# Kernel tuning notes

Hardware: AMD Instinct MI355X
Metric: run time of the kernel (lower is better)

## Reference

```python
import jax, jax.numpy as jnp
import numpy as np

DIM = 2048
N_HEADS = 32
N_KV_HEADS = 4
HEAD_DIM = DIM // N_HEADS  # 64


def _rope_tables(T, head_dim, dtype):
    inv_freq = 1.0 / (10000.0 ** (jnp.arange(0, head_dim, 2, dtype=jnp.float32) / head_dim))
    t = jnp.arange(T, dtype=jnp.float32)
    freqs = jnp.einsum('i,j->ij', t, inv_freq)           # [T, head_dim/2]
    emb = jnp.concatenate([freqs, freqs], axis=-1)        # [T, head_dim]
    return jnp.cos(emb).astype(dtype), jnp.sin(emb).astype(dtype)


def _rotate_half(x):
    d = x.shape[-1] // 2
    return jnp.concatenate([-x[..., d:], x[..., :d]], axis=-1)


def setup_inputs() -> dict:
    key = jax.random.key(0)
    kx, kq, kk, kv, ko = jax.random.split(key, 5)
    s = 1.0 / np.sqrt(DIM)
    return {
        'x': jax.random.normal(kx, (2, 2048, DIM), dtype=jnp.float32),
        'wq': jax.random.normal(kq, (DIM, DIM), dtype=jnp.float32) * s,
        'wk': jax.random.normal(kk, (DIM, DIM // 8), dtype=jnp.float32) * s,
        'wv': jax.random.normal(kv, (DIM, DIM // 8), dtype=jnp.float32) * s,
        'wo': jax.random.normal(ko, (DIM, DIM), dtype=jnp.float32) * s,
    }


def reference(x, wq, wk, wv, wo):
    B, T, C = x.shape
    q = (x @ wq).reshape(B, T, N_HEADS, HEAD_DIM).transpose(0, 2, 1, 3)      # [B,H,T,D]
    k = (x @ wk).reshape(B, T, N_KV_HEADS, HEAD_DIM).transpose(0, 2, 1, 3)   # [B,Hkv,T,D]
    v = (x @ wv).reshape(B, T, N_KV_HEADS, HEAD_DIM).transpose(0, 2, 1, 3)

    cos, sin = _rope_tables(T, HEAD_DIM, x.dtype)  # [T,D]
    q = q * cos + _rotate_half(q) * sin
    k = k * cos + _rotate_half(k) * sin

    rep = N_HEADS // N_KV_HEADS
    k = jnp.repeat(k, rep, axis=1)  # [B,H,T,D]
    v = jnp.repeat(v, rep, axis=1)

    scale = 1.0 / np.sqrt(HEAD_DIM)
    scores = jnp.einsum('bhqd,bhkd->bhqk', q, k) * scale
    causal = jnp.tril(jnp.ones((T, T), dtype=bool))
    scores = jnp.where(causal, scores, jnp.finfo(scores.dtype).min)
    attn = jax.nn.softmax(scores, axis=-1)
    out = jnp.einsum('bhqk,bhkd->bhqd', attn, v)
    out = out.transpose(0, 2, 1, 3).reshape(B, T, C)
    return out @ wo
```

## Files before the change

kernel.cpp:

```cpp
#include <hip/hip_runtime.h>
#include <hip/hip_bf16.h>
#include <stdint.h>

#define DIM 2048
#define TSEQ 2048
#define BATCH 2
#define NH 32
#define NKV 4
#define HD 64
#define MROWS (BATCH*TSEQ)
#define NQKV 2560

typedef __attribute__((ext_vector_type(4))) float f32x4;
typedef __attribute__((ext_vector_type(8))) __bf16 bf16x8;
typedef unsigned short ushort_t;

#define GLDS16(g, l) __builtin_amdgcn_global_load_lds( \
    (const __attribute__((address_space(1))) void*)(g), \
    (__attribute__((address_space(3))) void*)(l), 16, 0, 0)

__device__ __forceinline__ float bflo2f(unsigned int w) {
  union { unsigned int i; float f; } c; c.i = w << 16; return c.f;
}
__device__ __forceinline__ unsigned short f2bf(float f) {
  union { float f; unsigned int i; } c; c.f = f;
  unsigned int x = c.i;
  x += 0x7fffu + ((x >> 16) & 1u);
  return (unsigned short)(x >> 16);
}
__device__ __forceinline__ unsigned short f2bf_fast(float f) {
  union { float f; unsigned int i; } c; c.f = f;
  return (unsigned short)((c.i + 0x8000u) >> 16);
}

#define LOG1E4_D32 0.2878231366242557f
#define QSCALE 0.1803368801111243f
#define PREP_CAST 8192
#define PREP_TC   (PREP_CAST + 9216)
#define PREP_TAB  (PREP_TC + 256)

__global__ void prep_all(const float* __restrict__ x, ushort_t* __restrict__ xb,
                         const float* __restrict__ wq, const float* __restrict__ wk,
                         const float* __restrict__ wv, const float* __restrict__ wo,
                         ushort_t* __restrict__ wtq, ushort_t* __restrict__ woT,
                         float2* __restrict__ tab) {
  __shared__ float tile[32][33];
  const int bid = blockIdx.x;
  if (bid < PREP_CAST) {
    const int i = bid * 256 + threadIdx.x;
    const float4 v = ((const float4*)x)[i];
    uint2 p;
    p.x = (unsigned int)f2bf(v.x) | ((unsigned int)f2bf(v.y) << 16);
    p.y = (unsigned int)f2bf(v.z) | ((unsigned int)f2bf(v.w) << 16);
    ((uint2*)xb)[i] = p;
  } else if (bid < PREP_TC) {
    const int tb = bid - PREP_CAST;
    const int by = tb >> 6;
    const float* src; ushort_t* dst; int N, bnb;
    if (by < 64)      { src = wq; dst = wtq;                    N = DIM; bnb = by; }
    else if (by < 72) { src = wk; dst = wtq + (long)DIM  * DIM; N = 256; bnb = by - 64; }
    else if (by < 80) { src = wv; dst = wtq + (long)2304 * DIM; N = 256; bnb = by - 72; }
    else              { src = wo; dst = woT;                    N = DIM; bnb = by - 80; }
    const int bk = (tb & 63) * 32;
    const int bn = bnb * 32;
    const int tx = threadIdx.x & 31;
    const int ty = threadIdx.x >> 5;
#pragma unroll
    for (int p = 0; p < 4; p++) {
      const int r = ty + p * 8;
      tile[r][tx] = src[(long)(bk + r) * N + bn + tx];
    }
    __syncthreads();
#pragma unroll
    for (int p = 0; p < 4; p++) {
      const int r = ty + p * 8;
      dst[(long)(bn + r) * DIM + bk + tx] = f2bf(tile[tx][r]);
    }
  } else {
    const int i = (bid - PREP_TC) * 256 + threadIdx.x;
    const int t = i >> 5, d = i & 31;
    const float ang = (float)t * __expf(-(float)d * LOG1E4_D32);
    float s_, c_;
    __sincosf(ang, &s_, &c_);
    tab[i] = make_float2(c_, s_);
  }
}

template<int EPI>
__global__ __launch_bounds__(256, 4) void gemm_bt(
    const ushort_t* __restrict__ A, const ushort_t* __restrict__ BT,
    int M, int N, int K,
    float* __restrict__ Cf, ushort_t* __restrict__ Cq,
    ushort_t* __restrict__ Ck, ushort_t* __restrict__ Cv,
    const float2* __restrict__ tab)
{
  __shared__ __align__(16) ushort_t As[128][64];
  __shared__ __align__(16) ushort_t Bs[128][64];
  const int tid  = threadIdx.x;
  const int lane = tid & 63;
  const int wid  = tid >> 6;
  const int wm   = wid >> 1, wn = wid & 1;
  const int l8   = lane >> 3;
  const int c8   = (lane & 7) * 8;

  const int nwg = (int)(gridDim.x * gridDim.y);
  const int bid = (int)(blockIdx.y * gridDim.x + blockIdx.x);
  const int swz = (bid & 7) * (nwg >> 3) + (bid >> 3);
  const int bx  = swz & 31;
  const int by  = swz >> 5;

  const long abase = (long)bx * 128 * K;
  const long bbase = (long)by * 128 * K;
  const int rsel = lane & 15;
  const int koff = (lane >> 4) * 8;
  f32x4 acc[4][4] = {};

  for (int k0 = 0; k0 < K; k0 += 64) {
    __syncthreads();
#pragma unroll
    for (int i = 0; i < 4; i++) {
      const int r0 = wid * 32 + i * 8;
      GLDS16(&A [abase + (long)(r0 + l8) * K + k0 + c8], &As[r0][0]);
      GLDS16(&BT[bbase + (long)(r0 + l8) * K + k0 + c8], &Bs[r0][0]);
    }
    __syncthreads();
#pragma unroll
    for (int kk = 0; kk < 64; kk += 32) {
      bf16x8 af[4], bfr[4];
#pragma unroll
      for (int m = 0; m < 4; m++) af[m]  = *(const bf16x8*)(&As[wm*64 + m*16 + rsel][kk + koff]);
#pragma unroll
      for (int n = 0; n < 4; n++) bfr[n] = *(const bf16x8*)(&Bs[wn*64 + n*16 + rsel][kk + koff]);
#pragma unroll
      for (int m = 0; m < 4; m++)
#pragma unroll
        for (int n = 0; n < 4; n++)
          acc[m][n] = __builtin_amdgcn_mfma_f32_16x16x32_bf16(af[m], bfr[n], acc[m][n], 0, 0, 0);
    }
  }

  const int rbase = bx * 128 + wm * 64 + (lane >> 4) * 4;
  const int l15e  = lane & 15;

  if (EPI == 1) {
    const int cbase = by * 128 + wn * 64 + l15e;
#pragma unroll
    for (int m = 0; m < 4; m++)
#pragma unroll
      for (int n = 0; n < 4; n++) {
        const int gn = cbase + n * 16;
#pragma unroll
        for (int j = 0; j < 4; j++)
          Cf[(long)(rbase + m * 16 + j) * N + gn] = acc[m][n][j];
      }
  } else {
    const int colbase = by * 128 + wn * 64;
    if (colbase >= DIM + 256) {
#pragma unroll
      for (int m = 0; m < 4; m++) {
        const int gm0 = rbase + m * 16;
        const int b = gm0 >> 11;
        const int t = gm0 & (TSEQ - 1);
#pragma unroll
        for (int n = 0; n < 4; n++) {
          const int x = colbase + n * 16 + l15e - DIM;
          const int hkv = (x >> 6) & 3;
          const int d = x & 63;
          uint2 pk;
          pk.x = (unsigned int)f2bf(acc[m][n][0]) | ((unsigned int)f2bf(acc[m][n][1]) << 16);
          pk.y = (unsigned int)f2bf(acc[m][n][2]) | ((unsigned int)f2bf(acc[m][n][3]) << 16);
          *(uint2*)(&Cv[((long)(b * NKV + hkv) * HD + d) * TSEQ + t]) = pk;
        }
      }
    } else {
      const bool isQ = (colbase < DIM);
      const int hkv = (colbase - DIM) >> 6;
#pragma unroll
      for (int m = 0; m < 4; m++) {
#pragma unroll
        for (int j = 0; j < 4; j++) {
          const int gm = rbase + m * 16 + j;
          const int t = gm & (TSEQ - 1);
          const int b = gm >> 11;
          const float2 cs0 = tab[t * 32 + l15e];
          const float2 cs1 = tab[t * 32 + 16 + l15e];
          const float v0 = acc[m][0][j], v1 = acc[m][1][j];
          const float v2 = acc[m][2][j], v3 = acc[m][3][j];
          const float r0 = v0 * cs0.x - v2 * cs0.y;
          const float r2 = v2 * cs0.x + v0 * cs0.y;
          const float r1 = v1 * cs1.x - v3 * cs1.y;
          const float r3 = v3 * cs1.x + v1 * cs1.y;
          if (isQ) {
            const long base = (long)gm * DIM + colbase + l15e;
            Cq[base]      = f2bf(r0 * QSCALE);
            Cq[base + 16] = f2bf(r1 * QSCALE);
            Cq[base + 32] = f2bf(r2 * QSCALE);
            Cq[base + 48] = f2bf(r3 * QSCALE);
          } else {
            const long base = ((long)(b * NKV + hkv) * TSEQ + t) * HD + l15e;
            Ck[base]      = f2bf(r0);
            Ck[base + 16] = f2bf(r1);
            Ck[base + 32] = f2bf(r2);
            Ck[base + 48] = f2bf(r3);
          }
        }
      }
    }
  }
}

__global__ __launch_bounds__(256, 3) void attn_mfma(
    const ushort_t* __restrict__ q, const ushort_t* __restrict__ k,
    const ushort_t* __restrict__ vt, ushort_t* __restrict__ o)
{
  __shared__ __align__(16) ushort_t Ks[2][64][64];
  __shared__ __align__(16) ushort_t Vs[2][64][64];

  const int tid  = threadIdx.x;
  const int lane = tid & 63;
  const int wid  = tid >> 6;
  const int l15  = lane & 15;
  const int lg   = lane >> 4;
  const int od   = lg & 1;
  const int hi   = lg >> 1;
  const int sw   = l15 & 7;

  const int bh  = blockIdx.x & 63;
  const int qt  = (TSEQ / 128 - 1) - (blockIdx.x >> 6);
  const int h   = bh & (NH - 1);
  const int b   = bh >> 5;
  const int hkv = h >> 3;
  const int qw0 = qt * 128 + wid * 32;

  bf16x8 qf0c0, qf0c1, qf1c0, qf1c1;
  {
    const ushort_t* qp0 = q + ((long)(b * TSEQ) + qw0 + l15) * DIM + h * 64 + lg * 8;
    qf0c0 = *(const bf16x8*)(qp0);
    qf0c1 = *(const bf16x8*)(qp0 + 32);
    const ushort_t* qp1 = qp0 + 16 * DIM;
    qf1c0 = *(const bf16x8*)(qp1);
    qf1c1 = *(const bf16x8*)(qp1 + 32);
  }

  const ushort_t* kb_ = k  + (long)(b * NKV + hkv) * TSEQ * HD;
  const ushort_t* vb_ = vt + (long)(b * NKV + hkv) * HD * TSEQ;

  float lH0 = 0.f, lH1 = 0.f;
  f32x4 oH0[4] = {}, oH1[4] = {};

  const int srow = tid >> 2;
  const int sgc  = (tid & 3) * 16;
  const int g0   = 2 * (tid & 3);
  const int slc0 = ((g0    ) ^ (srow & 7)) * 8;
  const int slc1 = ((g0 + 1) ^ (srow & 7)) * 8;

  const int gv0 = ((0 + 2 * od + hi) ^ sw) * 8;
  const int gv1 = ((4 + 2 * od + hi) ^ sw) * 8;

  const int nkv = 2 * qt + 2;

  *(uint4*)(&Ks[0][srow][slc0]) = *(const uint4*)(&kb_[(long)srow * HD + sgc]);
  *(uint4*)(&Ks[0][srow][slc1]) = *(const uint4*)(&kb_[(long)srow * HD + sgc + 8]);
  *(uint4*)(&Vs[0][srow][slc0]) = *(const uint4*)(&vb_[(long)srow * TSEQ + sgc]);
  *(uint4*)(&Vs[0][srow][slc1]) = *(const uint4*)(&vb_[(long)srow * TSEQ + sgc + 8]);
  int cur = 0;

  union packu { unsigned int u[4]; bf16x8 v; };

#define PK(ST, KT, UA, UB, LL) { \
    const float p0 = exp2f(ST[KT][0]); \
    const float p1 = exp2f(ST[KT][1]); \
    const float p2 = exp2f(ST[KT][2]); \
    const float p3 = exp2f(ST[KT][3]); \
    LL += (p0 + p1) + (p2 + p3); \
    asm("v_cvt_pk_bf16_f32 %0, %1, %2" : "=v"(UA) : "v"(p0), "v"(p1)); \
    asm("v_cvt_pk_bf16_f32 %0, %1, %2" : "=v"(UB) : "v"(p2), "v"(p3)); \
  }

#define PACK_HALF(ST, LL, TT0, TT1) { \
    unsigned int u00, u01, u10, u11, u20, u21, u30, u31; \
    PK(ST, 0, u00, u01, LL) \
    PK(ST, 1, u10, u11, LL) \
    PK(ST, 2, u20, u21, LL) \
    PK(ST, 3, u30, u31, LL) \
    const unsigned int r00 = __shfl_xor((int)(od ? u00 : u10), 16, 64); \
    const unsigned int r01 = __shfl_xor((int)(od ? u01 : u11), 16, 64); \
    const unsigned int r10 = __shfl_xor((int)(od ? u20 : u30), 16, 64); \
    const unsigned int r11 = __shfl_xor((int)(od ? u21 : u31), 16, 64); \
    TT0.u[0] = od ? r00 : u00;  TT0.u[1] = od ? r01 : u01; \
    TT0.u[2] = od ? u10 : r00;  TT0.u[3] = od ? u11 : r01; \
    TT1.u[0] = od ? r10 : u20;  TT1.u[1] = od ? r11 : u21; \
    TT1.u[2] = od ? u30 : r10;  TT1.u[3] = od ? u31 : r11; \
  }

#define MASK_ST(ST, Q0) { \
    const int qg = (Q0) + l15; \
    _Pragma("unroll") \
    for (int kt = 0; kt < 4; kt++) { \
      const int kg0 = kb0 + kt * 16 + lg * 4; \
      _Pragma("unroll") \
      for (int j = 0; j < 4; j++) { \
        if (kg0 + j > qg) ST[kt][j] = -1e30f; \
      } \
    } \
  }

  for (int kbv = 0; kbv < nkv; kbv++) {
    const int kb0 = kbv * 64;
    const bool pf = (kbv + 1 < nkv);
    uint4 kr0 = {}, kr1 = {}, vr0 = {}, vr1 = {};
    if (pf) {
      kr0 = *(const uint4*)(&kb_[(long)(kb0 + 64 + srow) * HD + sgc]);
      kr1 = *(const uint4*)(&kb_[(long)(kb0 + 64 + srow) * HD + sgc + 8]);
      vr0 = *(const uint4*)(&vb_[(long)srow * TSEQ + kb0 + 64 + sgc]);
      vr1 = *(const uint4*)(&vb_[(long)srow * TSEQ + kb0 + 64 + sgc + 8]);
    }
    asm volatile("s_waitcnt lgkmcnt(0)\n\ts_barrier" ::: "memory");

    const bool a1 = (kb0 <= qw0 + 31);
    if (a1) {
      const bool a0 = (kb0 <= qw0 + 15);

      bf16x8 kfa[4], kfb[4];
#pragma unroll
      for (int kt = 0; kt < 4; kt++) {
        kfa[kt] = *(const bf16x8*)(&Ks[cur][kt * 16 + l15][((0 + lg) ^ sw) * 8]);
        kfb[kt] = *(const bf16x8*)(&Ks[cur][kt * 16 + l15][((4 + lg) ^ sw) * 8]);
      }

      f32x4 st1[4] = {};
      __builtin_amdgcn_s_setprio(1);
#pragma unroll
      for (int kt = 0; kt < 4; kt++) {
        st1[kt] = __builtin_amdgcn_mfma_f32_16x16x32_bf16(kfa[kt], qf1c0, st1[kt], 0, 0, 0);
        st1[kt] = __builtin_amdgcn_mfma_f32_16x16x32_bf16(kfb[kt], qf1c1, st1[kt], 0, 0, 0);
      }
      __builtin_amdgcn_s_setprio(0);
      f32x4 st0[4] = {};
      if (a0) {
        __builtin_amdgcn_s_setprio(1);
#pragma unroll
        for (int kt = 0; kt < 4; kt++) {
          st0[kt] = __builtin_amdgcn_mfma_f32_16x16x32_bf16(kfa[kt], qf0c0, st0[kt], 0, 0, 0);
          st0[kt] = __builtin_amdgcn_mfma_f32_16x16x32_bf16(kfb[kt], qf0c1, st0[kt], 0, 0, 0);
        }
        __builtin_amdgcn_s_setprio(0);
      }

      if (kb0 + 63 > qw0 + 16) MASK_ST(st1, qw0 + 16)
      if (a0 && kb0 + 63 > qw0) MASK_ST(st0, qw0)

      packu T0H1, T1H1, T0H0, T1H0;
      PACK_HALF(st1, lH1, T0H1, T1H1)
      if (a0) PACK_HALF(st0, lH0, T0H0, T1H0)

      bf16x8 vfa[4], vfb[4];
#pragma unroll
      for (int nt = 0; nt < 4; nt++) {
        vfa[nt] = *(const bf16x8*)(&Vs[cur][nt * 16 + l15][gv0]);
        vfb[nt] = *(const bf16x8*)(&Vs[cur][nt * 16 + l15][gv1]);
      }

      __builtin_amdgcn_s_setprio(1);
#pragma unroll
      for (int nt = 0; nt < 4; nt++)
        oH1[nt] = __builtin_amdgcn_mfma_f32_16x16x32_bf16(T0H1.v, vfa[nt], oH1[nt], 0, 0, 0);
#pragma unroll
      for (int nt = 0; nt < 4; nt++)
        oH1[nt] = __builtin_amdgcn_mfma_f32_16x16x32_bf16(T1H1.v, vfb[nt], oH1[nt], 0, 0, 0);
      __builtin_amdgcn_s_setprio(0);
      if (a0) {
        __builtin_amdgcn_s_setprio(1);
#pragma unroll
        for (int nt = 0; nt < 4; nt++)
          oH0[nt] = __builtin_amdgcn_mfma_f32_16x16x32_bf16(T0H0.v, vfa[nt], oH0[nt], 0, 0, 0);
#pragma unroll
        for (int nt = 0; nt < 4; nt++)
          oH0[nt] = __builtin_amdgcn_mfma_f32_16x16x32_bf16(T1H0.v, vfb[nt], oH0[nt], 0, 0, 0);
        __builtin_amdgcn_s_setprio(0);
      }
    }

    if (pf) {
      *(uint4*)(&Ks[cur ^ 1][srow][slc0]) = kr0;
      *(uint4*)(&Ks[cur ^ 1][srow][slc1]) = kr1;
      *(uint4*)(&Vs[cur ^ 1][srow][slc0]) = vr0;
      *(uint4*)(&Vs[cur ^ 1][srow][slc1]) = vr1;
    }
    cur ^= 1;
  }
#undef MASK_ST
#undef PACK_HALF
#undef PK

  {
    float lc = lH0;
    lc += __shfl_xor(lc, 16, 64);
    lc += __shfl_xor(lc, 32, 64);
    const long orow = (long)(b * TSEQ) + qw0;
#pragma unroll
    for (int j = 0; j < 4; j++) {
      const float inv = 1.f / __shfl(lc, (lane & 48) | (lg * 4 + j), 64);
#pragma unroll
      for (int nt = 0; nt < 4; nt++)
        o[(orow + lg * 4 + j) * DIM + h * 64 + nt * 16 + l15] = f2bf_fast(oH0[nt][j] * inv);
    }
  }
  {
    float lc = lH1;
    lc += __shfl_xor(lc, 16, 64);
    lc += __shfl_xor(lc, 32, 64);
    const long orow = (long)(b * TSEQ) + qw0 + 16;
#pragma unroll
    for (int j = 0; j < 4; j++) {
      const float inv = 1.f / __shfl(lc, (lane & 48) | (lg * 4 + j), 64);
#pragma unroll
      for (int nt = 0; nt < 4; nt++)
        o[(orow + lg * 4 + j) * DIM + h * 64 + nt * 16 + l15] = f2bf_fast(oH1[nt][j] * inv);
    }
  }
}

extern "C" void kernel_launch(void* const* d_in, const int* in_sizes, int n_in,
                              void* d_out, int out_size, void* d_ws, size_t ws_size,
                              hipStream_t stream) {
  const float* x  = (const float*)d_in[0];
  const float* wq = (const float*)d_in[1];
  const float* wk = (const float*)d_in[2];
  const float* wv = (const float*)d_in[3];
  const float* wo = (const float*)d_in[4];
  float* out = (float*)d_out;

  ushort_t* ws = (ushort_t*)d_ws;
  const long NXB = (long)MROWS * DIM;
  ushort_t* xb   = ws;
  ushort_t* wtq  = xb  + NXB;
  ushort_t* woT  = wtq + (long)NQKV * DIM;
  ushort_t* qws  = woT + (long)DIM * DIM;
  ushort_t* kws  = qws + NXB;
  ushort_t* vtws = kws + (long)BATCH * NKV * TSEQ * HD;
  ushort_t* aws  = vtws + (long)BATCH * NKV * TSEQ * HD;
  float2*   tab  = (float2*)(aws + NXB);

  prep_all<<<PREP_TAB, 256, 0, stream>>>(x, xb, wq, wk, wv, wo, wtq, woT, tab);

  gemm_bt<0><<<dim3(32, 20), 256, 0, stream>>>(xb, wtq, MROWS, NQKV, DIM,
                                               nullptr, qws, kws, vtws, tab);

  attn_mfma<<<BATCH * NH * (TSEQ / 128), 256, 0, stream>>>(qws, kws, vtws, aws);

  gemm_bt<1><<<dim3(32, 16), 256, 0, stream>>>(aws, woT, MROWS, DIM, DIM,
                                               out, nullptr, nullptr, nullptr, nullptr);
}
```

Before: 202.7 us.

## Double-buffer GEMM LDS tiles and use raw v_exp_f32 in attention softmax

```diff
diff --git a/kernel.cpp b/kernel.cpp
--- a/kernel.cpp
+++ b/kernel.cpp
@@ -31,6 +31,9 @@
 __device__ __forceinline__ unsigned short f2bf_fast(float f) {
   union { float f; unsigned int i; } c; c.f = f;
   return (unsigned short)((c.i + 0x8000u) >> 16);
+}
+__device__ __forceinline__ float fexp2(float x) {
+  float r; asm("v_exp_f32 %0, %1" : "=v"(r) : "v"(x)); return r;
 }
 
 #define LOG1E4_D32 0.2878231366242557f
@@ -87,15 +90,15 @@
 }
 
 template<int EPI>
-__global__ __launch_bounds__(256, 4) void gemm_bt(
+__global__ __launch_bounds__(256, 2) void gemm_bt(
     const ushort_t* __restrict__ A, const ushort_t* __restrict__ BT,
     int M, int N, int K,
     float* __restrict__ Cf, ushort_t* __restrict__ Cq,
     ushort_t* __restrict__ Ck, ushort_t* __restrict__ Cv,
     const float2* __restrict__ tab)
 {
-  __shared__ __align__(16) ushort_t As[128][64];
-  __shared__ __align__(16) ushort_t Bs[128][64];
+  __shared__ __align__(16) ushort_t As[2][128][64];
+  __shared__ __align__(16) ushort_t Bs[2][128][64];
   const int tid  = threadIdx.x;
   const int lane = tid & 63;
   const int wid  = tid >> 6;
@@ -115,29 +118,36 @@
   const int koff = (lane >> 4) * 8;
   f32x4 acc[4][4] = {};
 
+#define STAGE(BUF, KK0) { \
+    _Pragma("unroll") \
+    for (int i = 0; i < 4; i++) { \
+      const int r0 = wid * 32 + i * 8; \
+      GLDS16(&A [abase + (long)(r0 + l8) * K + (KK0) + c8], &As[BUF][r0][0]); \
+      GLDS16(&BT[bbase + (long)(r0 + l8) * K + (KK0) + c8], &Bs[BUF][r0][0]); \
+    } }
+
+  STAGE(0, 0)
+  int cur = 0;
+
   for (int k0 = 0; k0 < K; k0 += 64) {
-    __syncthreads();
-#pragma unroll
-    for (int i = 0; i < 4; i++) {
-      const int r0 = wid * 32 + i * 8;
-      GLDS16(&A [abase + (long)(r0 + l8) * K + k0 + c8], &As[r0][0]);
-      GLDS16(&BT[bbase + (long)(r0 + l8) * K + k0 + c8], &Bs[r0][0]);
-    }
-    __syncthreads();
+    asm volatile("s_waitcnt vmcnt(0) lgkmcnt(0)\n\ts_barrier" ::: "memory");
+    if (k0 + 64 < K) STAGE(cur ^ 1, k0 + 64)
 #pragma unroll
     for (int kk = 0; kk < 64; kk += 32) {
       bf16x8 af[4], bfr[4];
 #pragma unroll
-      for (int m = 0; m < 4; m++) af[m]  = *(const bf16x8*)(&As[wm*64 + m*16 + rsel][kk + koff]);
-#pragma unroll
-      for (int n = 0; n < 4; n++) bfr[n] = *(const bf16x8*)(&Bs[wn*64 + n*16 + rsel][kk + koff]);
+      for (int m = 0; m < 4; m++) af[m]  = *(const bf16x8*)(&As[cur][wm*64 + m*16 + rsel][kk + koff]);
+#pragma unroll
+      for (int n = 0; n < 4; n++) bfr[n] = *(const bf16x8*)(&Bs[cur][wn*64 + n*16 + rsel][kk + koff]);
 #pragma unroll
       for (int m = 0; m < 4; m++)
 #pragma unroll
         for (int n = 0; n < 4; n++)
           acc[m][n] = __builtin_amdgcn_mfma_f32_16x16x32_bf16(af[m], bfr[n], acc[m][n], 0, 0, 0);
     }
-  }
+    cur ^= 1;
+  }
+#undef STAGE
 
   const int rbase = bx * 128 + wm * 64 + (lane >> 4) * 4;
   const int l15e  = lane & 15;
@@ -268,10 +278,10 @@
   union packu { unsigned int u[4]; bf16x8 v; };
 
 #define PK(ST, KT, UA, UB, LL) { \
-    const float p0 = exp2f(ST[KT][0]); \
-    const float p1 = exp2f(ST[KT][1]); \
-    const float p2 = exp2f(ST[KT][2]); \
-    const float p3 = exp2f(ST[KT][3]); \
+    const float p0 = fexp2(ST[KT][0]); \
+    const float p1 = fexp2(ST[KT][1]); \
+    const float p2 = fexp2(ST[KT][2]); \
+    const float p3 = fexp2(ST[KT][3]); \
     LL += (p0 + p1) + (p2 + p3); \
     asm("v_cvt_pk_bf16_f32 %0, %1, %2" : "=v"(UA) : "v"(p0), "v"(p1)); \
     asm("v_cvt_pk_bf16_f32 %0, %1, %2" : "=v"(UB) : "v"(p2), "v"(p3)); \
```

Result: slower. 228.5 us (+12.7%).
